# Kernel optimization log

Hardware: AMD Instinct MI355X
Metric: run time of the kernel (lower is better)

The kernel has to match this reference:

```python
import jax, jax.numpy as jnp
import numpy as np

N_TOTAL = 1_000_000
B = 50_000
K = 32
D = 128


def setup_inputs() -> dict:
    key = jax.random.key(0)
    ks = jax.random.split(key, 10)
    return {
        "node_ids": jax.random.randint(ks[0], (B,), 0, N_TOTAL, dtype=jnp.int64 if jax.config.read('jax_enable_x64') else jnp.int32),
        "emb_table": jax.random.normal(ks[1], (N_TOTAL, D), dtype=jnp.float32),
        "offline_nbr_ids": jax.random.randint(ks[2], (N_TOTAL, K), 0, N_TOTAL, dtype=jnp.int64 if jax.config.read('jax_enable_x64') else jnp.int32),
        "offline_nbr_weights": jax.random.uniform(ks[3], (N_TOTAL, K), dtype=jnp.float32),
        "Wn_w": jax.random.normal(ks[4], (D, D), dtype=jnp.float32) / np.sqrt(D),
        "Wn_b": jax.random.normal(ks[5], (D,), dtype=jnp.float32) * 0.01,
        "Ws_w": jax.random.normal(ks[6], (D, D), dtype=jnp.float32) / np.sqrt(D),
        "Ws_b": jax.random.normal(ks[7], (D,), dtype=jnp.float32) * 0.01,
        "Wc_w": jax.random.normal(ks[8], (D, D), dtype=jnp.float32) / np.sqrt(D),
        "Wc_b": jax.random.normal(ks[9], (D,), dtype=jnp.float32) * 0.01,
    }


def reference(node_ids, emb_table, offline_nbr_ids, offline_nbr_weights,
              Wn_w, Wn_b, Ws_w, Ws_b, Wc_w, Wc_b):
    x_self = emb_table[node_ids]                       # [B, D]
    nbr_ids = offline_nbr_ids[node_ids]                # [B, K]
    nbr_w = offline_nbr_weights[node_ids]              # [B, K]
    nbr_embs = emb_table[nbr_ids]                      # [B, K, D]
    weighted = jnp.einsum('bkd,bk->bd', nbr_embs, nbr_w)  # gather + weighted reduce
    z_nbr = weighted @ Wn_w.T + Wn_b                   # [B, D]
    z_self = x_self @ Ws_w.T + Ws_b                    # [B, D]
    z = jax.nn.relu((z_nbr + z_self) @ Wc_w.T + Wc_b)
    return z
```

## Files before the change

kernel.cpp:

```cpp
#include <hip/hip_runtime.h>
#include <hip/hip_bf16.h>

#define D_DIM 128
#define K_NBR 32
#define NU 4
#define NWAVES 16
#define TPB (NWAVES * 64)
#define NBLK 256


__device__ __forceinline__ float bfu_lo(unsigned int w) {
    union { unsigned int i; float f; } v; v.i = w << 16; return v.f;
}
__device__ __forceinline__ float bfu_hi(unsigned int w) {
    union { unsigned int i; float f; } v; v.i = w & 0xffff0000u; return v.f;
}

__global__ void pinsage_precompute(const float* __restrict__ Wn_w, const float* __restrict__ Wn_b,
                                   const float* __restrict__ Ws_w, const float* __restrict__ Ws_b,
                                   const float* __restrict__ Wc_w, const float* __restrict__ Wc_b,
                                   unsigned short* __restrict__ GT2, float* __restrict__ bb) {
    const int d = threadIdx.x;
    const int b = blockIdx.x;
    if (b < 2 * D_DIM) {
        const int j = b;
        const float* Wsrc = (j < D_DIM) ? Wn_w : Ws_w;
        const int jj = j & (D_DIM - 1);
        float acc = 0.f;
        #pragma unroll 8
        for (int k = 0; k < D_DIM; ++k)
            acc += Wc_w[d * D_DIM + k] * Wsrc[k * D_DIM + jj];
        __hip_bfloat16 hb = __float2bfloat16(acc);
        unsigned short us = *reinterpret_cast<unsigned short*>(&hb);
        GT2[(((j >> 1) * D_DIM) + d) * 2 + (j & 1)] = us;
    } else {
        float acc = Wc_b[d];
        #pragma unroll 8
        for (int k = 0; k < D_DIM; ++k)
            acc += Wc_w[d * D_DIM + k] * (Wn_b[k] + Ws_b[k]);
        bb[d] = acc;
    }
}

__global__ __launch_bounds__(TPB, 4) void pinsage_main(
    const int* __restrict__ node_ids,
    const float* __restrict__ emb,
    const int* __restrict__ nbr_ids,
    const float* __restrict__ nbr_w,
    const unsigned short* __restrict__ GT2,
    const float* __restrict__ bbg,
    float* __restrict__ out,
    int B) {

    __shared__ unsigned short sGT[2 * D_DIM * D_DIM];
    __shared__ float sU[NWAVES][NU][2 * D_DIM];
    __shared__ int   sId[NWAVES][NU][K_NBR];
    __shared__ float sW[NWAVES][NU][K_NBR];

    const int tid = threadIdx.x;

    {
        const uint4* src = reinterpret_cast<const uint4*>(GT2);
        uint4* dst = reinterpret_cast<uint4*>(sGT);
        #pragma unroll
        for (int i = 0; i < 4; ++i)
            dst[tid + i * TPB] = src[tid + i * TPB];
    }
    __syncthreads();

    const int wave = tid >> 6;
    const int lane = tid & 63;
    const int h = lane >> 5;
    const int c = lane & 31;

    const float2 bbv = *reinterpret_cast<const float2*>(&bbg[2 * lane]);

    const int nGroups = (B + NU - 1) / NU;
    const int gstride = gridDim.x * NWAVES;

    for (int g = blockIdx.x * NWAVES + wave; g < nGroups; g += gstride) {
        const int base = g * NU;

        #pragma unroll
        for (int p = 0; p < 2; ++p) {
            const int i = 2 * p + h;
            const int n = base + i;
            const int nid = (n < B) ? node_ids[n] : 0;
            const size_t rb = (size_t)nid * K_NBR;
            sId[wave][i][c] = nbr_ids[rb + c];
            sW[wave][i][c]  = nbr_w[rb + c];
            const float4 xs = reinterpret_cast<const float4*>(emb + (size_t)nid * D_DIM)[c];
            *reinterpret_cast<float4*>(&sU[wave][i][D_DIM + 4 * c]) = xs;
        }

        #pragma unroll
        for (int p = 0; p < 2; ++p) {
            const int i = 2 * p + h;
            float4 a0 = make_float4(0.f, 0.f, 0.f, 0.f);
            float4 a1 = make_float4(0.f, 0.f, 0.f, 0.f);
            #pragma unroll 4
            for (int k = 0; k < K_NBR; k += 2) {
                const int id0 = sId[wave][i][k];
                const int id1 = sId[wave][i][k + 1];
                const float w0 = sW[wave][i][k];
                const float w1 = sW[wave][i][k + 1];
                const float4 r0 = reinterpret_cast<const float4*>(emb + (size_t)id0 * D_DIM)[c];
                const float4 r1 = reinterpret_cast<const float4*>(emb + (size_t)id1 * D_DIM)[c];
                a0.x = fmaf(w0, r0.x, a0.x); a0.y = fmaf(w0, r0.y, a0.y);
                a0.z = fmaf(w0, r0.z, a0.z); a0.w = fmaf(w0, r0.w, a0.w);
                a1.x = fmaf(w1, r1.x, a1.x); a1.y = fmaf(w1, r1.y, a1.y);
                a1.z = fmaf(w1, r1.z, a1.z); a1.w = fmaf(w1, r1.w, a1.w);
            }
            a0.x += a1.x; a0.y += a1.y; a0.z += a1.z; a0.w += a1.w;
            *reinterpret_cast<float4*>(&sU[wave][i][4 * c]) = a0;
        }

        float acc[NU][2];
        #pragma unroll
        for (int n = 0; n < NU; ++n) { acc[n][0] = 0.f; acc[n][1] = 0.f; }

        const unsigned short* gtp = &sGT[4 * lane];
        #pragma unroll 4
        for (int j2 = 0; j2 < D_DIM; ++j2) {
            const uint2 gw = *reinterpret_cast<const uint2*>(gtp + j2 * 256);
            const float g00 = bfu_lo(gw.x), g01 = bfu_hi(gw.x);
            const float g10 = bfu_lo(gw.y), g11 = bfu_hi(gw.y);
            #pragma unroll
            for (int n = 0; n < NU; ++n) {
                const float2 uu = *reinterpret_cast<const float2*>(&sU[wave][n][2 * j2]);
                acc[n][0] = fmaf(g00, uu.x, fmaf(g01, uu.y, acc[n][0]));
                acc[n][1] = fmaf(g10, uu.x, fmaf(g11, uu.y, acc[n][1]));
            }
        }

        #pragma unroll
        for (int n = 0; n < NU; ++n) {
            const int node = base + n;
            if (node < B) {
                float2 r;
                r.x = fmaxf(acc[n][0] + bbv.x, 0.f);
                r.y = fmaxf(acc[n][1] + bbv.y, 0.f);
                *reinterpret_cast<float2*>(&out[(size_t)node * D_DIM + 2 * lane]) = r;
            }
        }
    }
}

extern "C" void kernel_launch(void* const* d_in, const int* in_sizes, int n_in,
                              void* d_out, int out_size, void* d_ws, size_t ws_size,
                              hipStream_t stream) {
    const int*   node_ids = (const int*)  d_in[0];
    const float* emb      = (const float*)d_in[1];
    const int*   nbr_ids  = (const int*)  d_in[2];
    const float* nbr_w    = (const float*)d_in[3];
    const float* Wn_w     = (const float*)d_in[4];
    const float* Wn_b     = (const float*)d_in[5];
    const float* Ws_w     = (const float*)d_in[6];
    const float* Ws_b     = (const float*)d_in[7];
    const float* Wc_w     = (const float*)d_in[8];
    const float* Wc_b     = (const float*)d_in[9];
    const int B = in_sizes[0];

    unsigned short* GT2 = (unsigned short*)d_ws;
    float* bb = (float*)((char*)d_ws + 65536);
    float* out = (float*)d_out;

    pinsage_precompute<<<2 * D_DIM + 1, D_DIM, 0, stream>>>(Wn_w, Wn_b, Ws_w, Ws_b, Wc_w, Wc_b, GT2, bb);
    pinsage_main<<<NBLK, TPB, 0, stream>>>(node_ids, emb, nbr_ids, nbr_w, GT2, bb, out, B);
}
```

Measured before the change: 166.0 us.

## Read fused weight matrix from global/L2 instead of LDS to raise occupancy

The main kernel no longer stages the 64KB bf16 fused weight matrix in shared memory. It reads the matrix directly from global memory, relayouted so each lane loads a uint4 covering four input columns and two outputs. Dropping the LDS copy and raising launch bounds to 8 blocks per CU with 512 blocks is meant to increase occupancy and hide the latency of the random embedding gathers. The neighbor loop is unrolled to four loads in flight, and the precompute kernel caches Wc in padded shared memory. The cost is repeated global or L2 weight reads per group and register pressure under the tighter launch bounds.

```diff
diff --git a/kernel.cpp b/kernel.cpp
--- a/kernel.cpp
+++ b/kernel.cpp
@@ -6,7 +6,7 @@
 #define NU 4
 #define NWAVES 16
 #define TPB (NWAVES * 64)
-#define NBLK 256
+#define NBLK 512
 
 
 __device__ __forceinline__ float bfu_lo(unsigned int w) {
@@ -19,9 +19,24 @@
 __global__ void pinsage_precompute(const float* __restrict__ Wn_w, const float* __restrict__ Wn_b,
                                    const float* __restrict__ Ws_w, const float* __restrict__ Ws_b,
                                    const float* __restrict__ Wc_w, const float* __restrict__ Wc_b,
-                                   unsigned short* __restrict__ GT2, float* __restrict__ bb) {
+                                   unsigned short* __restrict__ GT4, float* __restrict__ bb) {
+    __shared__ float sWc[D_DIM * 129];
     const int d = threadIdx.x;
     const int b = blockIdx.x;
+
+    {
+        const float4* src = reinterpret_cast<const float4*>(Wc_w);
+        #pragma unroll
+        for (int i = 0; i < 32; ++i) {
+            const float4 v = src[d + i * D_DIM];
+            const int e = 4 * (d + i * D_DIM);
+            const int r = e >> 7, c0 = e & 127;
+            float* dst = &sWc[r * 129 + c0];
+            dst[0] = v.x; dst[1] = v.y; dst[2] = v.z; dst[3] = v.w;
+        }
+    }
+    __syncthreads();
+
     if (b < 2 * D_DIM) {
         const int j = b;
         const float* Wsrc = (j < D_DIM) ? Wn_w : Ws_w;
@@ -29,51 +44,42 @@
         float acc = 0.f;
         #pragma unroll 8
         for (int k = 0; k < D_DIM; ++k)
-            acc += Wc_w[d * D_DIM + k] * Wsrc[k * D_DIM + jj];
+            acc += sWc[d * 129 + k] * Wsrc[k * D_DIM + jj];
         __hip_bfloat16 hb = __float2bfloat16(acc);
         unsigned short us = *reinterpret_cast<unsigned short*>(&hb);
-        GT2[(((j >> 1) * D_DIM) + d) * 2 + (j & 1)] = us;
+        const int q = j >> 2, r = j & 3;
+        GT4[(((q * 64 + (d >> 1)) * 2 + (d & 1)) * 4) + r] = us;
     } else {
         float acc = Wc_b[d];
         #pragma unroll 8
         for (int k = 0; k < D_DIM; ++k)
-            acc += Wc_w[d * D_DIM + k] * (Wn_b[k] + Ws_b[k]);
+            acc += sWc[d * 129 + k] * (Wn_b[k] + Ws_b[k]);
         bb[d] = acc;
     }
 }
 
-__global__ __launch_bounds__(TPB, 4) void pinsage_main(
+__global__ __launch_bounds__(TPB, 8) void pinsage_main(
     const int* __restrict__ node_ids,
     const float* __restrict__ emb,
     const int* __restrict__ nbr_ids,
     const float* __restrict__ nbr_w,
-    const unsigned short* __restrict__ GT2,
+    const unsigned short* __restrict__ GT4,
     const float* __restrict__ bbg,
     float* __restrict__ out,
     int B) {
 
-    __shared__ unsigned short sGT[2 * D_DIM * D_DIM];
     __shared__ float sU[NWAVES][NU][2 * D_DIM];
     __shared__ int   sId[NWAVES][NU][K_NBR];
     __shared__ float sW[NWAVES][NU][K_NBR];
 
     const int tid = threadIdx.x;
-
-    {
-        const uint4* src = reinterpret_cast<const uint4*>(GT2);
-        uint4* dst = reinterpret_cast<uint4*>(sGT);
-        #pragma unroll
-        for (int i = 0; i < 4; ++i)
-            dst[tid + i * TPB] = src[tid + i * TPB];
-    }
-    __syncthreads();
-
     const int wave = tid >> 6;
     const int lane = tid & 63;
     const int h = lane >> 5;
     const int c = lane & 31;
 
     const float2 bbv = *reinterpret_cast<const float2*>(&bbg[2 * lane]);
+    const uint4* Gp = reinterpret_cast<const uint4*>(GT4) + lane;
 
     const int nGroups = (B + NU - 1) / NU;
     const int gstride = gridDim.x * NWAVES;
@@ -98,18 +104,27 @@
             const int i = 2 * p + h;
             float4 a0 = make_float4(0.f, 0.f, 0.f, 0.f);
             float4 a1 = make_float4(0.f, 0.f, 0.f, 0.f);
-            #pragma unroll 4
-            for (int k = 0; k < K_NBR; k += 2) {
+            for (int k = 0; k < K_NBR; k += 4) {
                 const int id0 = sId[wave][i][k];
                 const int id1 = sId[wave][i][k + 1];
+                const int id2 = sId[wave][i][k + 2];
+                const int id3 = sId[wave][i][k + 3];
                 const float w0 = sW[wave][i][k];
                 const float w1 = sW[wave][i][k + 1];
+                const float w2 = sW[wave][i][k + 2];
+                const float w3 = sW[wave][i][k + 3];
                 const float4 r0 = reinterpret_cast<const float4*>(emb + (size_t)id0 * D_DIM)[c];
                 const float4 r1 = reinterpret_cast<const float4*>(emb + (size_t)id1 * D_DIM)[c];
+                const float4 r2 = reinterpret_cast<const float4*>(emb + (size_t)id2 * D_DIM)[c];
+                const float4 r3 = reinterpret_cast<const float4*>(emb + (size_t)id3 * D_DIM)[c];
                 a0.x = fmaf(w0, r0.x, a0.x); a0.y = fmaf(w0, r0.y, a0.y);
                 a0.z = fmaf(w0, r0.z, a0.z); a0.w = fmaf(w0, r0.w, a0.w);
                 a1.x = fmaf(w1, r1.x, a1.x); a1.y = fmaf(w1, r1.y, a1.y);
                 a1.z = fmaf(w1, r1.z, a1.z); a1.w = fmaf(w1, r1.w, a1.w);
+                a0.x = fmaf(w2, r2.x, a0.x); a0.y = fmaf(w2, r2.y, a0.y);
+                a0.z = fmaf(w2, r2.z, a0.z); a0.w = fmaf(w2, r2.w, a0.w);
+                a1.x = fmaf(w3, r3.x, a1.x); a1.y = fmaf(w3, r3.y, a1.y);
+                a1.z = fmaf(w3, r3.z, a1.z); a1.w = fmaf(w3, r3.w, a1.w);
             }
             a0.x += a1.x; a0.y += a1.y; a0.z += a1.z; a0.w += a1.w;
             *reinterpret_cast<float4*>(&sU[wave][i][4 * c]) = a0;
@@ -119,17 +134,18 @@
         #pragma unroll
         for (int n = 0; n < NU; ++n) { acc[n][0] = 0.f; acc[n][1] = 0.f; }
 
-        const unsigned short* gtp = &sGT[4 * lane];
-        #pragma unroll 4
-        for (int j2 = 0; j2 < D_DIM; ++j2) {
-            const uint2 gw = *reinterpret_cast<const uint2*>(gtp + j2 * 256);
+        #pragma unroll 2
+        for (int q = 0; q < 64; ++q) {
+            const uint4 gw = Gp[q * 64];
             const float g00 = bfu_lo(gw.x), g01 = bfu_hi(gw.x);
-            const float g10 = bfu_lo(gw.y), g11 = bfu_hi(gw.y);
+            const float g02 = bfu_lo(gw.y), g03 = bfu_hi(gw.y);
+            const float g10 = bfu_lo(gw.z), g11 = bfu_hi(gw.z);
+            const float g12 = bfu_lo(gw.w), g13 = bfu_hi(gw.w);
             #pragma unroll
             for (int n = 0; n < NU; ++n) {
-                const float2 uu = *reinterpret_cast<const float2*>(&sU[wave][n][2 * j2]);
-                acc[n][0] = fmaf(g00, uu.x, fmaf(g01, uu.y, acc[n][0]));
-                acc[n][1] = fmaf(g10, uu.x, fmaf(g11, uu.y, acc[n][1]));
+                const float4 uu = *reinterpret_cast<const float4*>(&sU[wave][n][4 * q]);
+                acc[n][0] = fmaf(g00, uu.x, fmaf(g01, uu.y, fmaf(g02, uu.z, fmaf(g03, uu.w, acc[n][0]))));
+                acc[n][1] = fmaf(g10, uu.x, fmaf(g11, uu.y, fmaf(g12, uu.z, fmaf(g13, uu.w, acc[n][1]))));
             }
         }
 
@@ -161,10 +177,10 @@
     const float* Wc_b     = (const float*)d_in[9];
     const int B = in_sizes[0];
 
-    unsigned short* GT2 = (unsigned short*)d_ws;
+    unsigned short* GT4 = (unsigned short*)d_ws;
     float* bb = (float*)((char*)d_ws + 65536);
     float* out = (float*)d_out;
 
-    pinsage_precompute<<<2 * D_DIM + 1, D_DIM, 0, stream>>>(Wn_w, Wn_b, Ws_w, Ws_b, Wc_w, Wc_b, GT2, bb);
-    pinsage_main<<<NBLK, TPB, 0, stream>>>(node_ids, emb, nbr_ids, nbr_w, GT2, bb, out, B);
+    pinsage_precompute<<<2 * D_DIM + 1, D_DIM, 0, stream>>>(Wn_w, Wn_b, Ws_w, Ws_b, Wc_w, Wc_b, GT4, bb);
+    pinsage_main<<<NBLK, TPB, 0, stream>>>(node_ids, emb, nbr_ids, nbr_w, GT4, bb, out, B);
 }
```

Result: slower. 201.4 us (+21.3%).

## Add dynamic work stealing, double-buffered neighbor gathers, and LDS-staged Wc in precompute

Applied to the files above, without the earlier changes.

The main kernel now takes wave work groups from a global atomic counter instead of a fixed grid stride. The counter is seeded by the precompute kernel. The neighbor gather loop is restructured into 8 steps of 4 rows per node, with register double-buffering so the next step's loads are issued before the current step's FMAs. The precompute kernel stages Wc into padded shared memory to avoid strided global reads. These changes aim to balance tail imbalance and raise memory-level parallelism for the random embedding gathers, at the cost of higher register pressure, which could reduce occupancy.

```diff
diff --git a/kernel.cpp b/kernel.cpp
--- a/kernel.cpp
+++ b/kernel.cpp
@@ -7,6 +7,7 @@
 #define NWAVES 16
 #define TPB (NWAVES * 64)
 #define NBLK 256
+#define TOTAL_WAVES (NBLK * NWAVES)
 
 
 __device__ __forceinline__ float bfu_lo(unsigned int w) {
@@ -19,9 +20,25 @@
 __global__ void pinsage_precompute(const float* __restrict__ Wn_w, const float* __restrict__ Wn_b,
                                    const float* __restrict__ Ws_w, const float* __restrict__ Ws_b,
                                    const float* __restrict__ Wc_w, const float* __restrict__ Wc_b,
-                                   unsigned short* __restrict__ GT2, float* __restrict__ bb) {
+                                   unsigned short* __restrict__ GT2, float* __restrict__ bb,
+                                   int* __restrict__ cnt) {
+    __shared__ float sWc[D_DIM * 129];
     const int d = threadIdx.x;
     const int b = blockIdx.x;
+
+    {
+        const float4* src = reinterpret_cast<const float4*>(Wc_w);
+        #pragma unroll
+        for (int i = 0; i < 32; ++i) {
+            const float4 v = src[d + i * D_DIM];
+            const int e = 4 * (d + i * D_DIM);
+            const int r = e >> 7, c0 = e & 127;
+            float* dst = &sWc[r * 129 + c0];
+            dst[0] = v.x; dst[1] = v.y; dst[2] = v.z; dst[3] = v.w;
+        }
+    }
+    __syncthreads();
+
     if (b < 2 * D_DIM) {
         const int j = b;
         const float* Wsrc = (j < D_DIM) ? Wn_w : Ws_w;
@@ -29,7 +46,7 @@
         float acc = 0.f;
         #pragma unroll 8
         for (int k = 0; k < D_DIM; ++k)
-            acc += Wc_w[d * D_DIM + k] * Wsrc[k * D_DIM + jj];
+            acc += sWc[d * 129 + k] * Wsrc[k * D_DIM + jj];
         __hip_bfloat16 hb = __float2bfloat16(acc);
         unsigned short us = *reinterpret_cast<unsigned short*>(&hb);
         GT2[(((j >> 1) * D_DIM) + d) * 2 + (j & 1)] = us;
@@ -37,8 +54,9 @@
         float acc = Wc_b[d];
         #pragma unroll 8
         for (int k = 0; k < D_DIM; ++k)
-            acc += Wc_w[d * D_DIM + k] * (Wn_b[k] + Ws_b[k]);
+            acc += sWc[d * 129 + k] * (Wn_b[k] + Ws_b[k]);
         bb[d] = acc;
+        if (d == 0) *cnt = TOTAL_WAVES;
     }
 }
 
@@ -49,6 +67,7 @@
     const float* __restrict__ nbr_w,
     const unsigned short* __restrict__ GT2,
     const float* __restrict__ bbg,
+    int* __restrict__ cnt,
     float* __restrict__ out,
     int B) {
 
@@ -76,9 +95,10 @@
     const float2 bbv = *reinterpret_cast<const float2*>(&bbg[2 * lane]);
 
     const int nGroups = (B + NU - 1) / NU;
-    const int gstride = gridDim.x * NWAVES;
-
-    for (int g = blockIdx.x * NWAVES + wave; g < nGroups; g += gstride) {
+
+    int g = blockIdx.x * NWAVES + wave;
+
+    while (g < nGroups) {
         const int base = g * NU;
 
         #pragma unroll
@@ -93,26 +113,70 @@
             *reinterpret_cast<float4*>(&sU[wave][i][D_DIM + 4 * c]) = xs;
         }
 
+        int gn = nGroups;
+        if (lane == 0) gn = atomicAdd(cnt, 1);
+
+        float4 rb[2][2][4];
         #pragma unroll
         for (int p = 0; p < 2; ++p) {
             const int i = 2 * p + h;
-            float4 a0 = make_float4(0.f, 0.f, 0.f, 0.f);
-            float4 a1 = make_float4(0.f, 0.f, 0.f, 0.f);
-            #pragma unroll 4
-            for (int k = 0; k < K_NBR; k += 2) {
-                const int id0 = sId[wave][i][k];
-                const int id1 = sId[wave][i][k + 1];
-                const float w0 = sW[wave][i][k];
-                const float w1 = sW[wave][i][k + 1];
-                const float4 r0 = reinterpret_cast<const float4*>(emb + (size_t)id0 * D_DIM)[c];
-                const float4 r1 = reinterpret_cast<const float4*>(emb + (size_t)id1 * D_DIM)[c];
-                a0.x = fmaf(w0, r0.x, a0.x); a0.y = fmaf(w0, r0.y, a0.y);
-                a0.z = fmaf(w0, r0.z, a0.z); a0.w = fmaf(w0, r0.w, a0.w);
-                a1.x = fmaf(w1, r1.x, a1.x); a1.y = fmaf(w1, r1.y, a1.y);
-                a1.z = fmaf(w1, r1.z, a1.z); a1.w = fmaf(w1, r1.w, a1.w);
-            }
-            a0.x += a1.x; a0.y += a1.y; a0.z += a1.z; a0.w += a1.w;
-            *reinterpret_cast<float4*>(&sU[wave][i][4 * c]) = a0;
+            #pragma unroll
+            for (int kk = 0; kk < 4; ++kk) {
+                const int id = sId[wave][i][kk];
+                rb[0][p][kk] = reinterpret_cast<const float4*>(emb + (size_t)id * D_DIM)[c];
+            }
+        }
+        float4 accA[2], accB[2];
+        #pragma unroll
+        for (int p = 0; p < 2; ++p) {
+            accA[p] = make_float4(0.f, 0.f, 0.f, 0.f);
+            accB[p] = make_float4(0.f, 0.f, 0.f, 0.f);
+        }
+
+        #pragma unroll
+        for (int step = 0; step < 8; ++step) {
+            const int cur = step & 1;
+            const int kb = step * 4;
+            if (step < 7) {
+                #pragma unroll
+                for (int p = 0; p < 2; ++p) {
+                    const int i = 2 * p + h;
+                    #pragma unroll
+                    for (int kk = 0; kk < 4; ++kk) {
+                        const int id = sId[wave][i][kb + 4 + kk];
+                        rb[cur ^ 1][p][kk] = reinterpret_cast<const float4*>(emb + (size_t)id * D_DIM)[c];
+                    }
+                }
+            }
+            #pragma unroll
+            for (int p = 0; p < 2; ++p) {
+                const int i = 2 * p + h;
+                #pragma unroll
+                for (int kk = 0; kk < 4; ++kk) {
+                    const float w = sW[wave][i][kb + kk];
+                    const float4 r = rb[cur][p][kk];
+                    if (kk & 1) {
+                        accB[p].x = fmaf(w, r.x, accB[p].x);
+                        accB[p].y = fmaf(w, r.y, accB[p].y);
+                        accB[p].z = fmaf(w, r.z, accB[p].z);
+                        accB[p].w = fmaf(w, r.w, accB[p].w);
+                    } else {
+                        accA[p].x = fmaf(w, r.x, accA[p].x);
+                        accA[p].y = fmaf(w, r.y, accA[p].y);
+                        accA[p].z = fmaf(w, r.z, accA[p].z);
+                        accA[p].w = fmaf(w, r.w, accA[p].w);
+                    }
+                }
+            }
+        }
+
+        #pragma unroll
+        for (int p = 0; p < 2; ++p) {
+            const int i = 2 * p + h;
+            float4 s;
+            s.x = accA[p].x + accB[p].x; s.y = accA[p].y + accB[p].y;
+            s.z = accA[p].z + accB[p].z; s.w = accA[p].w + accB[p].w;
+            *reinterpret_cast<float4*>(&sU[wave][i][4 * c]) = s;
         }
 
         float acc[NU][2];
@@ -143,6 +207,8 @@
                 *reinterpret_cast<float2*>(&out[(size_t)node * D_DIM + 2 * lane]) = r;
             }
         }
+
+        g = __shfl(gn, 0);
     }
 }
 
@@ -162,9 +228,10 @@
     const int B = in_sizes[0];
 
     unsigned short* GT2 = (unsigned short*)d_ws;
-    float* bb = (float*)((char*)d_ws + 65536);
+    float* bb  = (float*)((char*)d_ws + 65536);
+    int*   cnt = (int*)  ((char*)d_ws + 66048);
     float* out = (float*)d_out;
 
-    pinsage_precompute<<<2 * D_DIM + 1, D_DIM, 0, stream>>>(Wn_w, Wn_b, Ws_w, Ws_b, Wc_w, Wc_b, GT2, bb);
-    pinsage_main<<<NBLK, TPB, 0, stream>>>(node_ids, emb, nbr_ids, nbr_w, GT2, bb, out, B);
-}
+    pinsage_precompute<<<2 * D_DIM + 1, D_DIM, 0, stream>>>(Wn_w, Wn_b, Ws_w, Ws_b, Wc_w, Wc_b, GT2, bb, cnt);
+    pinsage_main<<<NBLK, TPB, 0, stream>>>(node_ids, emb, nbr_ids, nbr_w, GT2, bb, cnt, out, B);
+}
```

Measured after the change: 222.9 us. 34.2% more time.

## Use atomic work-stealing for node groups and stage Wc in shared memory

Applied to the files above, without the earlier changes.

The main kernel's static grid-stride loop over 4-node groups is replaced by dynamic scheduling. Each wave fetches its next group index from a global atomic counter, which the precompute kernel initialises. This aims to even out load imbalance caused by variable gather latency across waves, at the cost of one atomic per group per wave. The precompute kernel also stages Wc_w into padded shared memory so its strided row reads no longer go to global memory.

```diff
diff --git a/kernel.cpp b/kernel.cpp
--- a/kernel.cpp
+++ b/kernel.cpp
@@ -7,6 +7,7 @@
 #define NWAVES 16
 #define TPB (NWAVES * 64)
 #define NBLK 256
+#define TOTAL_WAVES (NBLK * NWAVES)
 
 
 __device__ __forceinline__ float bfu_lo(unsigned int w) {
@@ -19,9 +20,25 @@
 __global__ void pinsage_precompute(const float* __restrict__ Wn_w, const float* __restrict__ Wn_b,
                                    const float* __restrict__ Ws_w, const float* __restrict__ Ws_b,
                                    const float* __restrict__ Wc_w, const float* __restrict__ Wc_b,
-                                   unsigned short* __restrict__ GT2, float* __restrict__ bb) {
+                                   unsigned short* __restrict__ GT2, float* __restrict__ bb,
+                                   int* __restrict__ cnt) {
+    __shared__ float sWc[D_DIM * 129];
     const int d = threadIdx.x;
     const int b = blockIdx.x;
+
+    {
+        const float4* src = reinterpret_cast<const float4*>(Wc_w);
+        #pragma unroll
+        for (int i = 0; i < 32; ++i) {
+            const float4 v = src[d + i * D_DIM];
+            const int e = 4 * (d + i * D_DIM);
+            const int r = e >> 7, c0 = e & 127;
+            float* dst = &sWc[r * 129 + c0];
+            dst[0] = v.x; dst[1] = v.y; dst[2] = v.z; dst[3] = v.w;
+        }
+    }
+    __syncthreads();
+
     if (b < 2 * D_DIM) {
         const int j = b;
         const float* Wsrc = (j < D_DIM) ? Wn_w : Ws_w;
@@ -29,7 +46,7 @@
         float acc = 0.f;
         #pragma unroll 8
         for (int k = 0; k < D_DIM; ++k)
-            acc += Wc_w[d * D_DIM + k] * Wsrc[k * D_DIM + jj];
+            acc += sWc[d * 129 + k] * Wsrc[k * D_DIM + jj];
         __hip_bfloat16 hb = __float2bfloat16(acc);
         unsigned short us = *reinterpret_cast<unsigned short*>(&hb);
         GT2[(((j >> 1) * D_DIM) + d) * 2 + (j & 1)] = us;
@@ -37,8 +54,9 @@
         float acc = Wc_b[d];
         #pragma unroll 8
         for (int k = 0; k < D_DIM; ++k)
-            acc += Wc_w[d * D_DIM + k] * (Wn_b[k] + Ws_b[k]);
+            acc += sWc[d * 129 + k] * (Wn_b[k] + Ws_b[k]);
         bb[d] = acc;
+        if (d == 0) *cnt = TOTAL_WAVES;
     }
 }
 
@@ -49,6 +67,7 @@
     const float* __restrict__ nbr_w,
     const unsigned short* __restrict__ GT2,
     const float* __restrict__ bbg,
+    int* __restrict__ cnt,
     float* __restrict__ out,
     int B) {
 
@@ -76,9 +95,10 @@
     const float2 bbv = *reinterpret_cast<const float2*>(&bbg[2 * lane]);
 
     const int nGroups = (B + NU - 1) / NU;
-    const int gstride = gridDim.x * NWAVES;
 
-    for (int g = blockIdx.x * NWAVES + wave; g < nGroups; g += gstride) {
+    int g = blockIdx.x * NWAVES + wave;
+
+    while (g < nGroups) {
         const int base = g * NU;
 
         #pragma unroll
@@ -92,6 +112,9 @@
             const float4 xs = reinterpret_cast<const float4*>(emb + (size_t)nid * D_DIM)[c];
             *reinterpret_cast<float4*>(&sU[wave][i][D_DIM + 4 * c]) = xs;
         }
+
+        int gn = nGroups;
+        if (lane == 0) gn = atomicAdd(cnt, 1);
 
         #pragma unroll
         for (int p = 0; p < 2; ++p) {
@@ -143,6 +166,8 @@
                 *reinterpret_cast<float2*>(&out[(size_t)node * D_DIM + 2 * lane]) = r;
             }
         }
+
+        g = __shfl(gn, 0);
     }
 }
 
@@ -162,9 +187,10 @@
     const int B = in_sizes[0];
 
     unsigned short* GT2 = (unsigned short*)d_ws;
-    float* bb = (float*)((char*)d_ws + 65536);
+    float* bb  = (float*)((char*)d_ws + 65536);
+    int*   cnt = (int*)  ((char*)d_ws + 66048);
     float* out = (float*)d_out;
 
-    pinsage_precompute<<<2 * D_DIM + 1, D_DIM, 0, stream>>>(Wn_w, Wn_b, Ws_w, Ws_b, Wc_w, Wc_b, GT2, bb);
-    pinsage_main<<<NBLK, TPB, 0, stream>>>(node_ids, emb, nbr_ids, nbr_w, GT2, bb, out, B);
+    pinsage_precompute<<<2 * D_DIM + 1, D_DIM, 0, stream>>>(Wn_w, Wn_b, Ws_w, Ws_b, Wc_w, Wc_b, GT2, bb, cnt);
+    pinsage_main<<<NBLK, TPB, 0, stream>>>(node_ids, emb, nbr_ids, nbr_w, GT2, bb, cnt, out, B);
 }
```

Result: slower. 223.3 us (+34.5%).
